# Kernel tuning notes

Hardware: AMD Instinct MI355X
Metric: run time of the kernel (lower is better)

## Reference

```python
import jax, jax.numpy as jnp
import numpy as np

D_MODEL = 1024
N_HEAD = 16
D_HEAD = D_MODEL // N_HEAD
FFN_HIDDEN = 4096
NEG_INF = -1e30


def sinusoid_pos_emb(pos_seq, d_model):
    # pos_seq: [K] descending relative positions; returns [K, d_model]
    inv_freq = 1.0 / (10000.0 ** (jnp.arange(0, d_model, 2, dtype=jnp.float32) / d_model))
    ang = pos_seq[:, None] * inv_freq[None, :]
    return jnp.concatenate([jnp.sin(ang), jnp.cos(ang)], axis=-1)


def rel_shift(x):
    # x: [B, H, Q, K] -> Transformer-XL relative shift
    b, h, q, k = x.shape
    x = jnp.pad(x, ((0, 0), (0, 0), (0, 0), (1, 0)))
    x = x.reshape(b, h, k + 1, q)[:, :, 1:, :].reshape(b, h, q, k)
    return x


def layer_norm(x, g, b, eps=1e-5):
    mu = jnp.mean(x, axis=-1, keepdims=True)
    var = jnp.var(x, axis=-1, keepdims=True)
    return (x - mu) * jax.lax.rsqrt(var + eps) * g + b


def setup_inputs() -> dict:
    key = jax.random.key(0)
    ks = jax.random.split(key, 20)
    B, T, M = 4, 2048, 2048
    s = 0.02
    inp = {
        "x": jax.random.normal(ks[0], (B, T, D_MODEL), jnp.float32),
        "mem": jax.random.normal(ks[1], (B, M, D_MODEL), jnp.float32),
        "Wq": jax.random.normal(ks[2], (D_MODEL, D_MODEL), jnp.float32) * s,
        "bq": jnp.zeros((D_MODEL,), jnp.float32),
        "Wk": jax.random.normal(ks[3], (D_MODEL, D_MODEL), jnp.float32) * s,
        "bk": jnp.zeros((D_MODEL,), jnp.float32),
        "Wv": jax.random.normal(ks[4], (D_MODEL, D_MODEL), jnp.float32) * s,
        "bv": jnp.zeros((D_MODEL,), jnp.float32),
        "Wo": jax.random.normal(ks[5], (D_MODEL, D_MODEL), jnp.float32) * s,
        "bo": jnp.zeros((D_MODEL,), jnp.float32),
        "Wr": jax.random.normal(ks[6], (D_MODEL, D_MODEL), jnp.float32) * s,
        "u": jax.random.normal(ks[7], (N_HEAD, D_HEAD), jnp.float32) * s,
        "v": jax.random.normal(ks[8], (N_HEAD, D_HEAD), jnp.float32) * s,
        "g1": jnp.ones((D_MODEL,), jnp.float32),
        "be1": jnp.zeros((D_MODEL,), jnp.float32),
        "g2": jnp.ones((D_MODEL,), jnp.float32),
        "be2": jnp.zeros((D_MODEL,), jnp.float32),
        "W1": jax.random.normal(ks[9], (D_MODEL, FFN_HIDDEN), jnp.float32) * s,
        "b1": jnp.zeros((FFN_HIDDEN,), jnp.float32),
        "W2": jax.random.normal(ks[10], (FFN_HIDDEN, D_MODEL), jnp.float32) * s,
        "b2": jnp.zeros((D_MODEL,), jnp.float32),
        "is_causal": 1,
    }
    return inp


def xl_attention(x, mem, Wq, bq, Wk, bk, Wv, bv, Wo, bo, Wr, u, v, is_causal):
    B, T, D = x.shape
    M = mem.shape[1]
    K = M + T
    c = jnp.concatenate([mem, x], axis=1)  # [B, K, D]
    q = (x @ Wq + bq).reshape(B, T, N_HEAD, D_HEAD)
    k = (c @ Wk + bk).reshape(B, K, N_HEAD, D_HEAD)
    vv = (c @ Wv + bv).reshape(B, K, N_HEAD, D_HEAD)
    pos_seq = jnp.arange(K - 1, -1, -1, dtype=jnp.float32)
    r = (sinusoid_pos_emb(pos_seq, D) @ Wr).reshape(K, N_HEAD, D_HEAD)
    # content term + relative-position term (Transformer-XL eq. A+C and B+D)
    AC = jnp.einsum('bihd,bjhd->bhij', q + u, k)
    BD = rel_shift(jnp.einsum('bihd,jhd->bhij', q + v, r))
    score = (AC + BD) * (1.0 / np.sqrt(D_HEAD))
    if is_causal:
        i = jnp.arange(T)[:, None]
        j = jnp.arange(K)[None, :]
        causal = (j <= i + M)  # query i may attend keys up to its own position
        score = jnp.where(causal[None, None], score, NEG_INF)
    attn = jax.nn.softmax(score, axis=-1)
    out = jnp.einsum('bhij,bjhd->bihd', attn, vv).reshape(B, T, D)
    return out @ Wo + bo


def reference(x, mem, Wq, bq, Wk, bk, Wv, bv, Wo, bo, Wr, u, v,
              g1, be1, g2, be2, W1, b1, W2, b2, is_causal):
    # dropout is identity at inference
    a = xl_attention(x, mem, Wq, bq, Wk, bk, Wv, bv, Wo, bo, Wr, u, v, is_causal)
    h = layer_norm(a + x, g1, be1)
    f = jax.nn.gelu(h @ W1 + b1) @ W2 + b2
    return layer_norm(f + h, g2, be2)
```

## Files before the change

### kernel.cpp

```cpp
#include <hip/hip_runtime.h>
#include <stdint.h>

typedef unsigned short u16;
typedef short s16x8 __attribute__((ext_vector_type(8)));
typedef unsigned short u16x4 __attribute__((ext_vector_type(4)));
typedef float f32x4 __attribute__((ext_vector_type(4)));

#define DEV static __device__ __forceinline__

DEV u16 f2b(float f) {
  union { float f; unsigned u; } v; v.f = f;
  unsigned r = v.u + 0x7fffu + ((v.u >> 16) & 1u);
  return (u16)(r >> 16);
}
DEV float b2f(u16 b) {
  union { unsigned u; float f; } v; v.u = ((unsigned)b) << 16; return v.f;
}
DEV unsigned pk_trunc(float a, float b) {
  return __builtin_amdgcn_perm(__float_as_uint(b), __float_as_uint(a), 0x07060302u);
}
DEV f32x4 MFMA16(s16x8 a, s16x8 b, f32x4 c) {
  return __builtin_amdgcn_mfma_f32_16x16x32_bf16(a, b, c, 0, 0, 0);
}
#define GLD_LDS16(gp, lp)                                                            \
  __builtin_amdgcn_global_load_lds((const __attribute__((address_space(1))) void*)(gp), \
                                   (__attribute__((address_space(3))) void*)(lp), 16, 0, 0)


__global__ __launch_bounds__(256) void wt_cast_t(const float* __restrict__ W,
                                                 u16* __restrict__ Wt, int Kd, int Nd) {
  __shared__ float tile[32][33];
  const int n0 = blockIdx.x * 32, k0 = blockIdx.y * 32;
  const int t = threadIdx.x;
#pragma unroll
  for (int p = 0; p < 4; ++p) {
    int idx = p * 256 + t; int r = idx >> 5, c = idx & 31;
    tile[r][c] = W[(long)(k0 + r) * Nd + n0 + c];
  }
  __syncthreads();
#pragma unroll
  for (int p = 0; p < 4; ++p) {
    int idx = p * 256 + t; int r = idx >> 5, c = idx & 31;
    Wt[(long)(n0 + r) * Kd + k0 + c] = f2b(tile[c][r]);
  }
}

__global__ __launch_bounds__(256) void build_cb(const float* __restrict__ x,
                                                const float* __restrict__ mem,
                                                u16* __restrict__ cb) {
  long idx = (long)blockIdx.x * 256 + threadIdx.x;
  long e4 = idx * 4;
  int b = (int)(e4 >> 22);
  long rem = e4 & ((1L << 22) - 1);
  int tok = (int)(rem >> 10);
  int d = (int)(rem & 1023);
  const float* src = (tok < 2048) ? &mem[((long)b * 2048 + tok) * 1024 + d]
                                  : &x[((long)b * 2048 + (tok - 2048)) * 1024 + d];
  float4 vv = *(const float4*)src;
  uint2 o;
  o.x = (unsigned)f2b(vv.x) | ((unsigned)f2b(vv.y) << 16);
  o.y = (unsigned)f2b(vv.z) | ((unsigned)f2b(vv.w) << 16);
  *(uint2*)&cb[e4] = o;
}

__global__ __launch_bounds__(256) void pos_emb(u16* __restrict__ pe) {
  const int d = blockIdx.x;
  const int e0 = threadIdx.x * 4;
  u16 o[4];
#pragma unroll
  for (int i = 0; i < 4; ++i) {
    int e = e0 + i;
    int f = (e < 512) ? e : (e - 512);
    float invf = expf(-(float)f * (9.210340371976184f / 512.f));
    float ang = (float)d * invf;
    o[i] = f2b((e < 512) ? sinf(ang) : cosf(ang));
  }
  uint2 pk; pk.x = (unsigned)o[0] | ((unsigned)o[1] << 16);
  pk.y = (unsigned)o[2] | ((unsigned)o[3] << 16);
  *(uint2*)&pe[(long)d * 1024 + e0] = pk;
}

#define EPI_BF16 0
#define EPI_F32 1
#define EPI_GELU 2
#define EPI_VT 3

template <int EPI, int QMAP>
__global__ __launch_bounds__(256) void gemm_bt(const u16* __restrict__ A,
                                               const u16* __restrict__ Bt,
                                               const float* __restrict__ bias,
                                               void* __restrict__ outp, int Ndim, int Kdim) {
  __shared__ __align__(16) u16 As[128 * 32];
  __shared__ __align__(16) u16 Bs[128 * 32];
  const int col0 = blockIdx.x * 128;
  const int row0 = blockIdx.y * 128;
  const int t = threadIdx.x;
  const int w = t >> 6, l = t & 63;
  const int wr = (w >> 1) * 64, wc = (w & 1) * 64;
  const int lr = l & 15, lk = (l >> 4) * 8;
  f32x4 acc[4][4];
#pragma unroll
  for (int m = 0; m < 4; ++m)
#pragma unroll
    for (int n = 0; n < 4; ++n) acc[m][n] = f32x4{0.f, 0.f, 0.f, 0.f};

  for (int k0 = 0; k0 < Kdim; k0 += 32) {
#pragma unroll
    for (int it = 0; it < 2; ++it) {
      int c = it * 256 + t;
      int r = c >> 2, e = (c & 3) * 8;
      long ga = row0 + r;
      if (QMAP) ga = ((ga >> 11) << 12) + 2048 + (ga & 2047);
      GLD_LDS16(A + ga * Kdim + k0 + e, &As[c * 8]);
      GLD_LDS16(Bt + (long)(col0 + r) * Kdim + k0 + e, &Bs[c * 8]);
    }
    __syncthreads();
    s16x8 af[4], bfv[4];
#pragma unroll
    for (int m = 0; m < 4; ++m) af[m] = *(const s16x8*)&As[(wr + m * 16 + lr) * 32 + lk];
#pragma unroll
    for (int n = 0; n < 4; ++n) bfv[n] = *(const s16x8*)&Bs[(wc + n * 16 + lr) * 32 + lk];
#pragma unroll
    for (int m = 0; m < 4; ++m)
#pragma unroll
      for (int n = 0; n < 4; ++n) acc[m][n] = MFMA16(af[m], bfv[n], acc[m][n]);
    __syncthreads();
  }

  const int lg = (l >> 4) * 4;
#pragma unroll
  for (int m = 0; m < 4; ++m) {
    int rbase = row0 + wr + m * 16 + lg;
#pragma unroll
    for (int n = 0; n < 4; ++n) {
      int gc = col0 + wc + n * 16 + lr;
      float bv = bias ? bias[gc] : 0.f;
#pragma unroll
      for (int rg = 0; rg < 4; ++rg) {
        int grow = rbase + rg;
        float vv = acc[m][n][rg] + bv;
        if (EPI == EPI_GELU) {
          float x3 = vv * vv * vv;
          vv = 0.5f * vv * (1.f + tanhf(0.7978845608028654f * (vv + 0.044715f * x3)));
        }
        if (EPI == EPI_F32) {
          ((float*)outp)[(long)grow * Ndim + gc] = vv;
        } else if (EPI == EPI_VT) {
          int bb = grow >> 12, tok = grow & 4095;
          int hh = gc >> 6, dd = gc & 63;
          ((u16*)outp)[((long)((bb * 16 + hh) * 64 + dd) << 12) + tok] = f2b(vv);
        } else {
          ((u16*)outp)[(long)grow * Ndim + gc] = f2b(vv);
        }
      }
    }
  }
}

#define SCALE_LOG2 0.18033688011111793f

__global__ __launch_bounds__(512, 4) void attn_fused(
    const u16* __restrict__ qg, const u16* __restrict__ kg, const u16* __restrict__ vTg,
    const u16* __restrict__ rg, const float* __restrict__ u, const float* __restrict__ vparam,
    const int* __restrict__ causal_p, u16* __restrict__ Og) {
  __shared__ __align__(16) u16 Ks[2][64 * 64];
  __shared__ __align__(16) u16 Vs[2][64 * 64];
  __shared__ __align__(16) u16 GPs[8][16 * 80];

  const int bh = blockIdx.x, b = bh >> 4, h = bh & 15;
  const int i0 = (int)(gridDim.y - 1 - blockIdx.y) * 128;
  const int t = threadIdx.x, w = t >> 6, l = t & 63;
  const int q = l & 15, g = l >> 4, lk = g * 8;
  const int causal = causal_p[0];

  const long kbase = ((long)b * 4096) * 1024 + h * 64;
  const long vbase = ((long)((b * 16 + h) * 64)) * 4096;

  const int irow = i0 + 16 * w + q;
  const u16* qp = qg + ((long)(b * 2048 + irow)) * 1024 + h * 64;
  s16x8 qlo = *(const s16x8*)(qp + lk);
  s16x8 qhi = *(const s16x8*)(qp + 32 + lk);
  s16x8 qu0, qu1, qv0, qv1;
#pragma unroll
  for (int j = 0; j < 8; ++j) {
    float a0 = b2f((u16)qlo[j]), a1 = b2f((u16)qhi[j]);
    float uu0 = u[h * 64 + lk + j], vv0 = vparam[h * 64 + lk + j];
    float uu1 = u[h * 64 + 32 + lk + j], vv1 = vparam[h * 64 + 32 + lk + j];
    qu0[j] = (short)f2b((a0 + uu0) * SCALE_LOG2); qv0[j] = (short)f2b((a0 + vv0) * SCALE_LOG2);
    qu1[j] = (short)f2b((a1 + uu1) * SCALE_LOG2); qv1[j] = (short)f2b((a1 + vv1) * SCALE_LOG2);
  }

  float lsum = 0.f;
  f32x4 oacc[4];
#pragma unroll
  for (int n = 0; n < 4; ++n) oacc[n] = f32x4{0.f, 0.f, 0.f, 0.f};

  u16* gpw = &GPs[w][0];
  const int kc0 = q * 64 + ((g ^ (q & 7)) << 3);
  const int kc1 = kc0 ^ 32;
  const int gq = q * 81 + 63;
  const int gst = q * 80 + 4 * g;
  const int pst = q * 72 + 4 * g;
  const int prd = q * 72 + lk;

  auto STAGE = [&](int j0s, int bufi) {
    int rrow = t >> 3, gch = (t & 7) ^ (rrow & 7);
    GLD_LDS16(kg + kbase + (long)(j0s + rrow) * 1024 + gch * 8, &Ks[bufi][t * 8]);
    GLD_LDS16(vTg + vbase + (long)rrow * 4096 + j0s + gch * 8, &Vs[bufi][t * 8]);
  };

  const int jmax = causal ? (2048 + i0 + 128) : 4096;
  const int nt = jmax >> 6;
  const int jlimit = 2048 + i0 + 16 * w + 15;
  STAGE(0, 0);
  int cur = 0;

  for (int ti = 0; ti < nt; ++ti) {
    const int j0 = ti << 6;
    asm volatile("s_waitcnt vmcnt(0)" ::: "memory");
    __syncthreads();
    if (ti + 1 < nt) STAGE((ti + 1) << 6, cur ^ 1);

    if (!causal || j0 <= jlimit) {
      const u16* ksp = &Ks[cur][0];
      const u16* vsp = &Vs[cur][0];

      const int dlo = 2048 + i0 + 16 * w - j0 - 63;
      s16x8 rf0[5], rf1[5];
#pragma unroll
      for (int tt = 0; tt < 5; ++tt) {
        int d = dlo + tt * 16 + q; d = min(max(d, 0), 4095);
        const u16* rp = rg + ((long)d << 10) + h * 64;
        rf0[tt] = *(const s16x8*)(rp + lk);
        rf1[tt] = *(const s16x8*)(rp + 32 + lk);
      }

      f32x4 sv[4];
      __builtin_amdgcn_s_setprio(1);
#pragma unroll
      for (int n = 0; n < 4; ++n) {
        s16x8 af0 = *(const s16x8*)&ksp[kc0 + n * 1024];
        s16x8 af1 = *(const s16x8*)&ksp[kc1 + n * 1024];
        f32x4 z = f32x4{0.f, 0.f, 0.f, 0.f};
        z = MFMA16(af0, qu0, z);
        z = MFMA16(af1, qu1, z);
        sv[n] = z;
      }
#pragma unroll
      for (int tt = 0; tt < 5; ++tt) {
        f32x4 z = f32x4{0.f, 0.f, 0.f, 0.f};
        z = MFMA16(rf0[tt], qv0, z);
        z = MFMA16(rf1[tt], qv1, z);
        uint2 gp2 = {pk_trunc(z[0], z[1]), pk_trunc(z[2], z[3])};
        *(u16x4*)&gpw[gst + tt * 16] = __builtin_bit_cast(u16x4, gp2);
      }
      __builtin_amdgcn_s_setprio(0);

      const bool need_mask = (causal != 0) && (j0 + 63 > 2048 + i0 + 16 * w);
#pragma unroll
      for (int n = 0; n < 4; ++n) {
#pragma unroll
        for (int r = 0; r < 4; ++r) {
          int j = 16 * n + 4 * g + r;
          float bd = b2f(gpw[gq - j]);
          float scv = sv[n][r] + bd;
          if (need_mask && (j0 + j > 2048 + irow)) scv = -3.0e38f;
          sv[n][r] = scv;
        }
      }
      float ls = 0.f;
#pragma unroll
      for (int n = 0; n < 4; ++n) {
        float p0 = __builtin_amdgcn_exp2f(sv[n][0]);
        float p1 = __builtin_amdgcn_exp2f(sv[n][1]);
        float p2 = __builtin_amdgcn_exp2f(sv[n][2]);
        float p3 = __builtin_amdgcn_exp2f(sv[n][3]);
        ls += (p0 + p1) + (p2 + p3);
        uint2 pp = {pk_trunc(p0, p1), pk_trunc(p2, p3)};
        *(u16x4*)&gpw[pst + n * 16] = __builtin_bit_cast(u16x4, pp);
      }
      lsum += ls;

      s16x8 pb0 = *(const s16x8*)&gpw[prd];
      s16x8 pb1 = *(const s16x8*)&gpw[prd + 32];
      __builtin_amdgcn_s_setprio(1);
#pragma unroll
      for (int n = 0; n < 4; ++n) {
        s16x8 va0 = *(const s16x8*)&vsp[kc0 + n * 1024];
        s16x8 va1 = *(const s16x8*)&vsp[kc1 + n * 1024];
        oacc[n] = MFMA16(va0, pb0, oacc[n]);
        oacc[n] = MFMA16(va1, pb1, oacc[n]);
      }
      __builtin_amdgcn_s_setprio(0);
    }
    cur ^= 1;
  }

  lsum += __shfl_xor(lsum, 16);
  lsum += __shfl_xor(lsum, 32);
  const float linv = 1.f / lsum;
  const long obase = (long)(b * 2048 + irow) * 1024 + h * 64;
#pragma unroll
  for (int n = 0; n < 4; ++n) {
    u16x4 ov = {f2b(oacc[n][0] * linv), f2b(oacc[n][1] * linv),
                f2b(oacc[n][2] * linv), f2b(oacc[n][3] * linv)};
    *(u16x4*)&Og[obase + n * 16 + 4 * g] = ov;
  }
}

template <int WRITE_BF16>
__global__ __launch_bounds__(256) void ln_res(const float* __restrict__ a,
                                              const float* __restrict__ resid,
                                              const float* __restrict__ g,
                                              const float* __restrict__ be,
                                              float* __restrict__ outf, u16* __restrict__ outb) {
  const int row = blockIdx.x;
  const int t = threadIdx.x;
  const long base = (long)row * 1024;
  float4 av = *(const float4*)&a[base + t * 4];
  float4 rv = *(const float4*)&resid[base + t * 4];
  float x0 = av.x + rv.x, x1 = av.y + rv.y, x2 = av.z + rv.z, x3 = av.w + rv.w;
  float s = x0 + x1 + x2 + x3;
  float q = x0 * x0 + x1 * x1 + x2 * x2 + x3 * x3;
#pragma unroll
  for (int d = 1; d < 64; d <<= 1) {
    s += __shfl_xor(s, d);
    q += __shfl_xor(q, d);
  }
  __shared__ float ss[4], sq[4];
  if ((t & 63) == 0) { ss[t >> 6] = s; sq[t >> 6] = q; }
  __syncthreads();
  s = ss[0] + ss[1] + ss[2] + ss[3];
  q = sq[0] + sq[1] + sq[2] + sq[3];
  float mu = s * (1.f / 1024.f);
  float var = q * (1.f / 1024.f) - mu * mu;
  float rstd = rsqrtf(var + 1e-5f);
  float4 gv = *(const float4*)&g[t * 4];
  float4 bv = *(const float4*)&be[t * 4];
  float y0 = (x0 - mu) * rstd * gv.x + bv.x;
  float y1 = (x1 - mu) * rstd * gv.y + bv.y;
  float y2 = (x2 - mu) * rstd * gv.z + bv.z;
  float y3 = (x3 - mu) * rstd * gv.w + bv.w;
  float4 ov = {y0, y1, y2, y3};
  *(float4*)&outf[base + t * 4] = ov;
  if (WRITE_BF16) {
    uint2 o;
    o.x = (unsigned)f2b(y0) | ((unsigned)f2b(y1) << 16);
    o.y = (unsigned)f2b(y2) | ((unsigned)f2b(y3) << 16);
    *(uint2*)&outb[base + t * 4] = o;
  }
}

extern "C" void kernel_launch(void* const* d_in, const int* in_sizes, int n_in, void* d_out,
                              int out_size, void* d_ws, size_t ws_size, hipStream_t stream) {
  const float* x = (const float*)d_in[0];
  const float* mem = (const float*)d_in[1];
  const float* Wq = (const float*)d_in[2];
  const float* bq = (const float*)d_in[3];
  const float* Wk = (const float*)d_in[4];
  const float* bk = (const float*)d_in[5];
  const float* Wv = (const float*)d_in[6];
  const float* bv = (const float*)d_in[7];
  const float* Wo = (const float*)d_in[8];
  const float* bo = (const float*)d_in[9];
  const float* Wr = (const float*)d_in[10];
  const float* u = (const float*)d_in[11];
  const float* vp = (const float*)d_in[12];
  const float* g1 = (const float*)d_in[13];
  const float* be1 = (const float*)d_in[14];
  const float* g2 = (const float*)d_in[15];
  const float* be2 = (const float*)d_in[16];
  const float* W1 = (const float*)d_in[17];
  const float* b1 = (const float*)d_in[18];
  const float* W2 = (const float*)d_in[19];
  const float* b2 = (const float*)d_in[20];
  const int* iscaus = (const int*)d_in[21];

  char* ws = (char*)d_ws;
  const size_t MB = 1024 * 1024;
  u16* WqT = (u16*)(ws + 0 * MB);
  u16* WkT = (u16*)(ws + 2 * MB);
  u16* WvT = (u16*)(ws + 4 * MB);
  u16* WoT = (u16*)(ws + 6 * MB);
  u16* WrT = (u16*)(ws + 8 * MB);
  u16* W1T = (u16*)(ws + 10 * MB);
  u16* W2T = (u16*)(ws + 18 * MB);
  u16* cb = (u16*)(ws + 26 * MB);
  float* proj = (float*)(ws + 26 * MB);
  u16* pe = (u16*)(ws + 58 * MB);
  u16* qb = (u16*)(ws + 66 * MB);
  u16* kb = (u16*)(ws + 82 * MB);
  u16* vT = (u16*)(ws + 114 * MB);
  u16* rb = (u16*)(ws + 146 * MB);
  u16* aO = (u16*)(ws + 154 * MB);
  u16* hb = (u16*)(ws + 154 * MB);
  u16* f1 = (u16*)(ws + 58 * MB);
  float* f2 = (float*)(ws + 122 * MB);
  (void)ws_size; (void)in_sizes; (void)n_in; (void)out_size;

  wt_cast_t<<<dim3(32, 32), 256, 0, stream>>>(Wq, WqT, 1024, 1024);
  wt_cast_t<<<dim3(32, 32), 256, 0, stream>>>(Wk, WkT, 1024, 1024);
  wt_cast_t<<<dim3(32, 32), 256, 0, stream>>>(Wv, WvT, 1024, 1024);
  wt_cast_t<<<dim3(32, 32), 256, 0, stream>>>(Wo, WoT, 1024, 1024);
  wt_cast_t<<<dim3(32, 32), 256, 0, stream>>>(Wr, WrT, 1024, 1024);
  wt_cast_t<<<dim3(128, 32), 256, 0, stream>>>(W1, W1T, 1024, 4096);
  wt_cast_t<<<dim3(32, 128), 256, 0, stream>>>(W2, W2T, 4096, 1024);

  build_cb<<<16384, 256, 0, stream>>>(x, mem, cb);
  pos_emb<<<4096, 256, 0, stream>>>(pe);

  gemm_bt<EPI_BF16, 1><<<dim3(8, 64), 256, 0, stream>>>(cb, WqT, bq, qb, 1024, 1024);
  gemm_bt<EPI_BF16, 0><<<dim3(8, 128), 256, 0, stream>>>(cb, WkT, bk, kb, 1024, 1024);
  gemm_bt<EPI_VT, 0><<<dim3(8, 128), 256, 0, stream>>>(cb, WvT, bv, vT, 1024, 1024);
  gemm_bt<EPI_BF16, 0><<<dim3(8, 32), 256, 0, stream>>>(pe, WrT, nullptr, rb, 1024, 1024);

  attn_fused<<<dim3(64, 16), 512, 0, stream>>>(qb, kb, vT, rb, u, vp, iscaus, aO);

  gemm_bt<EPI_F32, 0><<<dim3(8, 64), 256, 0, stream>>>(aO, WoT, bo, proj, 1024, 1024);
  ln_res<1><<<8192, 256, 0, stream>>>(proj, x, g1, be1, proj, hb);

  gemm_bt<EPI_GELU, 0><<<dim3(32, 64), 256, 0, stream>>>(hb, W1T, b1, f1, 4096, 1024);
  gemm_bt<EPI_F32, 0><<<dim3(8, 64), 256, 0, stream>>>(f1, W2T, b2, f2, 1024, 4096);
  ln_res<0><<<8192, 256, 0, stream>>>(f2, proj, g2, be2, (float*)d_out, nullptr);
}
```

Measured before the change: 1.105 ms.

## Stage relative-position rows through a shared LDS ring buffer

Previously each wave loaded its own 80 rows of the relative-position projection R straight from global memory on every key tile, which is largely redundant across the eight waves. Now the block cooperatively streams R rows into a three-slot, 64-row LDS ring with an XOR swizzle, and each wave reads its BD operands from LDS. This cuts redundant global traffic and the register pressure of holding the R fragments. In exchange it adds a second barrier per iteration so a slot is not overwritten while being read, and it drops the explicit vmcnt wait before the main barrier, which risks a race if the async LDS loads are not otherwise waited on.

```diff
diff --git a/kernel.cpp b/kernel.cpp
--- a/kernel.cpp
+++ b/kernel.cpp
@@ -165,7 +165,8 @@
     const int* __restrict__ causal_p, u16* __restrict__ Og) {
   __shared__ __align__(16) u16 Ks[2][64 * 64];
   __shared__ __align__(16) u16 Vs[2][64 * 64];
-  __shared__ __align__(16) u16 GPs[8][16 * 80];
+  __shared__ __align__(16) u16 Rs[192 * 64];
+  __shared__ __align__(16) u16 GPs[8][16 * 84];
 
   const int bh = blockIdx.x, b = bh >> 4, h = bh & 15;
   const int i0 = (int)(gridDim.y - 1 - blockIdx.y) * 128;
@@ -198,8 +199,8 @@
   u16* gpw = &GPs[w][0];
   const int kc0 = q * 64 + ((g ^ (q & 7)) << 3);
   const int kc1 = kc0 ^ 32;
-  const int gq = q * 81 + 63;
-  const int gst = q * 80 + 4 * g;
+  const int gq = q * 85 + 63;
+  const int gst = q * 84 + 4 * g;
   const int pst = q * 72 + 4 * g;
   const int prd = q * 72 + lk;
 
@@ -209,33 +210,36 @@
     GLD_LDS16(vTg + vbase + (long)rrow * 4096 + j0s + gch * 8, &Vs[bufi][t * 8]);
   };
 
+  auto STAGE_R = [&](int Dnew) {
+    int rr = t >> 3, c = t & 7;
+    int d = Dnew + rr;
+    int e = d + 768;
+    int sb = ((e >> 6) % 3) << 6;
+    int dc = min(max(d, 0), 4095);
+    GLD_LDS16(rg + ((long)dc << 10) + h * 64 + ((c ^ (rr & 7)) << 3),
+              &Rs[(sb + rr) * 64 + c * 8]);
+  };
+
   const int jmax = causal ? (2048 + i0 + 128) : 4096;
   const int nt = jmax >> 6;
   const int jlimit = 2048 + i0 + 16 * w + 15;
+
   STAGE(0, 0);
+  const int D00 = 2048 + i0;
+#pragma unroll
+  for (int k = 0; k < 3; ++k) STAGE_R(D00 - 64 + 64 * k);
   int cur = 0;
 
   for (int ti = 0; ti < nt; ++ti) {
     const int j0 = ti << 6;
-    asm volatile("s_waitcnt vmcnt(0)" ::: "memory");
     __syncthreads();
     if (ti + 1 < nt) STAGE((ti + 1) << 6, cur ^ 1);
 
-    if (!causal || j0 <= jlimit) {
+    const bool live = !causal || j0 <= jlimit;
+    f32x4 sv[4];
+    if (live) {
       const u16* ksp = &Ks[cur][0];
-      const u16* vsp = &Vs[cur][0];
-
-      const int dlo = 2048 + i0 + 16 * w - j0 - 63;
-      s16x8 rf0[5], rf1[5];
-#pragma unroll
-      for (int tt = 0; tt < 5; ++tt) {
-        int d = dlo + tt * 16 + q; d = min(max(d, 0), 4095);
-        const u16* rp = rg + ((long)d << 10) + h * 64;
-        rf0[tt] = *(const s16x8*)(rp + lk);
-        rf1[tt] = *(const s16x8*)(rp + 32 + lk);
-      }
-
-      f32x4 sv[4];
+
       __builtin_amdgcn_s_setprio(1);
 #pragma unroll
       for (int n = 0; n < 4; ++n) {
@@ -246,16 +250,30 @@
         z = MFMA16(af1, qu1, z);
         sv[n] = z;
       }
+      const int ebase = 2048 + i0 + 16 * w - j0 - 63 + q + 768;
 #pragma unroll
       for (int tt = 0; tt < 5; ++tt) {
+        int e = ebase + 16 * tt;
+        int slot = (((e >> 6) % 3) << 6) + (e & 63);
+        int co = slot * 64 + ((g ^ (e & 7)) << 3);
+        s16x8 r0 = *(const s16x8*)&Rs[co];
+        s16x8 r1 = *(const s16x8*)&Rs[co ^ 32];
         f32x4 z = f32x4{0.f, 0.f, 0.f, 0.f};
-        z = MFMA16(rf0[tt], qv0, z);
-        z = MFMA16(rf1[tt], qv1, z);
+        z = MFMA16(r0, qv0, z);
+        z = MFMA16(r1, qv1, z);
         uint2 gp2 = {pk_trunc(z[0], z[1]), pk_trunc(z[2], z[3])};
         *(u16x4*)&gpw[gst + tt * 16] = __builtin_bit_cast(u16x4, gp2);
       }
       __builtin_amdgcn_s_setprio(0);
-
+    }
+
+    asm volatile("" ::: "memory");
+    __builtin_amdgcn_s_barrier();
+    asm volatile("" ::: "memory");
+    if (ti + 1 < nt) STAGE_R(2048 + i0 - j0 - 128);
+
+    if (live) {
+      const u16* vsp = &Vs[cur][0];
       const bool need_mask = (causal != 0) && (j0 + 63 > 2048 + i0 + 16 * w);
 #pragma unroll
       for (int n = 0; n < 4; ++n) {
```

New measurement: 1.180 ms. 1.07x slower.
